# Performance work log

Hardware: AMD Instinct MI355X
Metric: run time of the kernel (lower is better)

The kernel has to match this reference:

```python
import jax, jax.numpy as jnp
import numpy as np

BS, H, NUM_JOB, NUM_OP, DK = 8, 16, 64, 64, 64
OPS_PER_JOB = 32
L = NUM_JOB * OPS_PER_JOB  # length_q = 2048; exactly L true slots per batch elem


def setup_inputs() -> dict:
    key = jax.random.key(0)
    k1, k2, k3 = jax.random.split(key, 3)
    q = jax.random.normal(k1, (BS, H, L, DK), dtype=jnp.float32)
    k = jax.random.normal(k2, (BS, H, L, DK), dtype=jnp.float32)
    v = jax.random.normal(k3, (BS, H, L, DK), dtype=jnp.float32)
    # ragged job->op mapping: first OPS_PER_JOB slots of each job are occupied
    op_mapping = jnp.tile((jnp.arange(NUM_OP) < OPS_PER_JOB)[None, None, :],
                          (BS, NUM_JOB, 1))  # (bs, num_job, num_op) bool
    # causal (lower-triangular) mask within each job
    tri = jnp.tril(jnp.ones((NUM_OP, NUM_OP), dtype=bool))
    triu_mask = jnp.tile(tri[None, None, :, :], (BS, NUM_JOB, 1, 1))
    return {"q": q, "k": k, "v": v, "op_mapping": op_mapping, "triu_mask": triu_mask}


def _rope_tables(num_op, dk):
    pos = jnp.arange(num_op, dtype=jnp.float32)
    i = jnp.arange(dk // 2, dtype=jnp.float32)
    theta = 1.0 / (10000.0 ** (2.0 * i / dk))
    ang = pos[:, None] * theta[None, :]                 # (num_op, dk/2)
    cos2 = jnp.repeat(jnp.cos(ang), 2, axis=-1)          # (num_op, dk) -> repeat_interleave(2)
    sin2 = jnp.repeat(jnp.sin(ang), 2, axis=-1)
    return cos2, sin2


def _rotate_half(x):
    xe = x[..., ::2]
    xo = x[..., 1::2]
    return jnp.stack([-xo, xe], axis=-1).reshape(x.shape)


def reference(q, k, v, op_mapping, triu_mask):
    bs, h, length_q, dk = q.shape
    _, num_job, num_op = op_mapping.shape
    flat_map = op_mapping.reshape(bs, num_job * num_op)  # (bs, J*O) bool
    # masked_scatter_ equivalent: true slot t (in flat row-major order) gets token cumsum-1
    pos = jnp.clip(jnp.cumsum(flat_map, axis=-1) - 1, 0, length_q - 1)  # (bs, J*O)
    idx = pos[:, None, :, None]  # broadcast over heads and dk

    def scatter_to_jobs(x):
        g = jnp.take_along_axis(x, idx, axis=2)                       # (bs,h,J*O,dk)
        g = jnp.where(flat_map[:, None, :, None], g, jnp.zeros((), x.dtype))
        return g.reshape(bs, h, num_job, num_op, dk)

    mq = scatter_to_jobs(q)
    mk = scatter_to_jobs(k)
    mv = scatter_to_jobs(v)

    # RoPE over the op axis
    cos2, sin2 = _rope_tables(num_op, dk)                             # (num_op, dk)
    mq = mq * cos2 + _rotate_half(mq) * sin2
    mk = mk * cos2 + _rotate_half(mk) * sin2

    score = jnp.einsum('bhjod,bhjpd->bhjop', mq, mk)                  # (bs,h,J,O,O)
    scale = 1.0 / jnp.sqrt(jnp.float32(dk))
    mask = triu_mask[:, None] & (score != 0)                          # compound mask
    s = jnp.where(mask, score * scale, -jnp.inf)
    invalid = jnp.sum(mask, axis=-1, keepdims=True) == 0              # empty rows
    s = jnp.where(invalid, jnp.float32(-1e9), s)
    w = jax.nn.softmax(s, axis=-1)
    out = jnp.einsum('bhjop,bhjpd->bhjod', w, mv)                     # (bs,h,J,O,dk)

    # gather back: out[matrix_mapping].reshape(bs,h,L,dk)
    out_flat = out.reshape(bs, h, num_job * num_op, dk)
    sel = jax.vmap(lambda m: jnp.nonzero(m, size=length_q)[0])(flat_map)  # (bs, L)
    tok = jnp.take_along_axis(out_flat, sel[:, None, :, None], axis=2)    # (bs,h,L,dk)
    # permute [0,2,1,3] then flatten heads: (bs, L, h*dk)
    return tok.transpose(0, 2, 1, 3).reshape(bs, length_q, h * dk)
```

## Files before the change

kernel.cpp:

```cpp
#include <hip/hip_runtime.h>
#include <hip/hip_bf16.h>


typedef _Float16 h8 __attribute__((ext_vector_type(8)));
typedef float f4 __attribute__((ext_vector_type(4)));
typedef unsigned short us8 __attribute__((ext_vector_type(8)));

__device__ __forceinline__ float bf2f(unsigned short u) {
    return __uint_as_float(((unsigned int)u) << 16);
}

__device__ __forceinline__ void load8f(const void* base, size_t idx, bool isbf, float o[8]) {
    if (isbf) {
        us8 v = *(const us8*)((const unsigned short*)base + idx);
#pragma unroll
        for (int t = 0; t < 8; ++t) o[t] = bf2f(v[t]);
    } else {
        const float* p = (const float*)base + idx;
        float4 a = *(const float4*)p;
        float4 b = *(const float4*)(p + 4);
        o[0] = a.x; o[1] = a.y; o[2] = a.z; o[3] = a.w;
        o[4] = b.x; o[5] = b.y; o[6] = b.z; o[7] = b.w;
    }
}

__device__ __forceinline__ float load1f(const void* base, size_t idx, bool isbf) {
    return isbf ? bf2f(((const unsigned short*)base)[idx])
                : ((const float*)base)[idx];
}

#define ROPE_LN_CONST 0.28782313662425575f

__global__ __launch_bounds__(256)
void attn_jobs(const void* __restrict__ qp, const void* __restrict__ kp,
               const void* __restrict__ vp, float* __restrict__ outp) {
    __shared__ float ps[4][32 * 33];

    const int tid  = threadIdx.x;
    const int wid  = tid >> 6;
    const int lane = tid & 63;
    const int lg   = lane >> 4;
    const int ln   = lane & 15;

    const int sub = blockIdx.x * 4 + wid;
    const int j = sub & 63;
    const int h = (sub >> 6) & 15;
    const int b = sub >> 10;

    unsigned int w0 = ((const unsigned int*)qp)[lane];
    unsigned int e8 = (w0 >> 7) & 0xFFu;
    bool hit = (e8 >= 96u) && (e8 <= 144u);
    const bool isbf = (__popcll(__ballot(hit)) >= 32);

    const size_t base = ((size_t)((b * 16 + h) * 2048 + j * 32)) * 64;

    h8 qf[2][2], kf[2][2];
#pragma unroll
    for (int ti = 0; ti < 2; ++ti) {
        const int r = ti * 16 + ln;
#pragma unroll
        for (int c = 0; c < 2; ++c) {
            const int dbase = c * 32 + lg * 8;
            float qa[8], ka[8];
            load8f(qp, base + (size_t)r * 64 + dbase, isbf, qa);
            load8f(kp, base + (size_t)r * 64 + dbase, isbf, ka);
#pragma unroll
            for (int t = 0; t < 4; ++t) {
                const int i = (dbase >> 1) + t;
                const float th = __expf(-(float)i * ROPE_LN_CONST);
                float sn, cs;
                __sincosf((float)r * th, &sn, &cs);
                const float qe = qa[2 * t], qo = qa[2 * t + 1];
                const float ke = ka[2 * t], ko = ka[2 * t + 1];
                qf[ti][c][2 * t]     = (_Float16)(qe * cs - qo * sn);
                qf[ti][c][2 * t + 1] = (_Float16)(qo * cs + qe * sn);
                kf[ti][c][2 * t]     = (_Float16)(ke * cs - ko * sn);
                kf[ti][c][2 * t + 1] = (_Float16)(ko * cs + ke * sn);
            }
        }
    }

    f4 sacc[2][2];
#pragma unroll
    for (int ti = 0; ti < 2; ++ti)
#pragma unroll
        for (int tj = 0; tj < 2; ++tj) {
            f4 acc = {0.f, 0.f, 0.f, 0.f};
            acc = __builtin_amdgcn_mfma_f32_16x16x32_f16(qf[ti][0], kf[tj][0], acc, 0, 0, 0);
            acc = __builtin_amdgcn_mfma_f32_16x16x32_f16(qf[ti][1], kf[tj][1], acc, 0, 0, 0);
            sacc[ti][tj] = acc;
        }

#pragma unroll
    for (int ti = 0; ti < 2; ++ti) {
#pragma unroll
        for (int reg = 0; reg < 4; ++reg) {
            const int row = ti * 16 + lg * 4 + reg;
            float s0 = sacc[ti][0][reg] * 0.125f;
            float s1 = sacc[ti][1][reg] * 0.125f;
            if (ln > row)      s0 = -INFINITY;
            if (16 + ln > row) s1 = -INFINITY;
            float m = fmaxf(s0, s1);
#pragma unroll
            for (int off = 8; off > 0; off >>= 1) m = fmaxf(m, __shfl_xor(m, off, 64));
            float p0 = __expf(s0 - m);
            float p1 = __expf(s1 - m);
            float l = p0 + p1;
#pragma unroll
            for (int off = 8; off > 0; off >>= 1) l += __shfl_xor(l, off, 64);
            const float linv = 1.0f / l;
            sacc[ti][0][reg] = p0 * linv;
            sacc[ti][1][reg] = p1 * linv;
        }
    }

    float* myps = ps[wid];
#pragma unroll
    for (int ti = 0; ti < 2; ++ti)
#pragma unroll
        for (int tj = 0; tj < 2; ++tj)
#pragma unroll
            for (int reg = 0; reg < 4; ++reg)
                myps[(ti * 16 + lg * 4 + reg) * 33 + tj * 16 + ln] = sacc[ti][tj][reg];
    __syncthreads();

    h8 paf[2];
#pragma unroll
    for (int ti = 0; ti < 2; ++ti)
#pragma unroll
        for (int t = 0; t < 8; ++t)
            paf[ti][t] = (_Float16)myps[(ti * 16 + ln) * 33 + lg * 8 + t];

    h8 vf[4];
#pragma unroll
    for (int tj = 0; tj < 4; ++tj)
#pragma unroll
        for (int t = 0; t < 8; ++t)
            vf[tj][t] = (_Float16)load1f(vp, base + (size_t)(lg * 8 + t) * 64 + tj * 16 + ln, isbf);

    f4 oacc[2][4];
#pragma unroll
    for (int ti = 0; ti < 2; ++ti)
#pragma unroll
        for (int tj = 0; tj < 4; ++tj) {
            f4 acc = {0.f, 0.f, 0.f, 0.f};
            oacc[ti][tj] = __builtin_amdgcn_mfma_f32_16x16x32_f16(paf[ti], vf[tj], acc, 0, 0, 0);
        }

#pragma unroll
    for (int ti = 0; ti < 2; ++ti)
#pragma unroll
        for (int reg = 0; reg < 4; ++reg) {
            const int row = ti * 16 + lg * 4 + reg;
            const size_t obase = ((size_t)b * 2048 + j * 32 + row) * 1024 + h * 64;
#pragma unroll
            for (int tj = 0; tj < 4; ++tj)
                outp[obase + tj * 16 + ln] = oacc[ti][tj][reg];
        }
}

extern "C" void kernel_launch(void* const* d_in, const int* in_sizes, int n_in,
                              void* d_out, int out_size, void* d_ws, size_t ws_size,
                              hipStream_t stream) {
    (void)in_sizes; (void)n_in; (void)d_ws; (void)ws_size; (void)out_size;
    const void* q = d_in[0];
    const void* k = d_in[1];
    const void* v = d_in[2];
    attn_jobs<<<2048, 256, 0, stream>>>(q, k, v, (float*)d_out);
}
```

Measured before the change: 225.6 us.

## Prefetch V before QK^T, store P as fp16 in LDS, drop block barrier

V is now loaded into raw registers before the QK^T MFMAs and softmax, so its global latency overlaps that compute instead of sitting after the softmax. The probability tile goes to LDS as fp16 with a padded stride, so each lane reads it back as a single vector of eight halves. The block-wide __syncthreads is replaced by a per-wave lgkmcnt wait, which relies on each wave using only its own LDS slice. Launch bounds request 4 blocks per CU and outputs are stored right after each MFMA, at the cost of 32 extra live registers for the prefetched V.

```diff
diff --git a/kernel.cpp b/kernel.cpp
--- a/kernel.cpp
+++ b/kernel.cpp
@@ -24,17 +24,12 @@
     }
 }
 
-__device__ __forceinline__ float load1f(const void* base, size_t idx, bool isbf) {
-    return isbf ? bf2f(((const unsigned short*)base)[idx])
-                : ((const float*)base)[idx];
-}
-
 #define ROPE_LN_CONST 0.28782313662425575f
 
-__global__ __launch_bounds__(256)
+__global__ __launch_bounds__(256, 4)
 void attn_jobs(const void* __restrict__ qp, const void* __restrict__ kp,
                const void* __restrict__ vp, float* __restrict__ outp) {
-    __shared__ float ps[4][32 * 33];
+    __shared__ alignas(16) _Float16 ps[4][32 * 40];
 
     const int tid  = threadIdx.x;
     const int wid  = tid >> 6;
@@ -49,8 +44,8 @@
 
     unsigned int w0 = ((const unsigned int*)qp)[lane];
     unsigned int e8 = (w0 >> 7) & 0xFFu;
-    bool hit = (e8 >= 96u) && (e8 <= 144u);
-    const bool isbf = (__popcll(__ballot(hit)) >= 32);
+    bool hitb = (e8 >= 96u) && (e8 <= 144u);
+    const bool isbf = (__popcll(__ballot(hitb)) >= 32);
 
     const size_t base = ((size_t)((b * 16 + h) * 2048 + j * 32)) * 64;
 
@@ -78,6 +73,23 @@
                 kf[ti][c][2 * t + 1] = (_Float16)(ko * cs + ke * sn);
             }
         }
+    }
+
+    unsigned int vr[32];
+    if (isbf) {
+#pragma unroll
+        for (int tj = 0; tj < 4; ++tj)
+#pragma unroll
+            for (int t = 0; t < 8; ++t)
+                vr[tj * 8 + t] = ((const unsigned short*)vp)
+                    [base + (size_t)(lg * 8 + t) * 64 + tj * 16 + ln];
+    } else {
+#pragma unroll
+        for (int tj = 0; tj < 4; ++tj)
+#pragma unroll
+            for (int t = 0; t < 8; ++t)
+                vr[tj * 8 + t] = ((const unsigned int*)vp)
+                    [base + (size_t)(lg * 8 + t) * 64 + tj * 16 + ln];
     }
 
     f4 sacc[2][2];
@@ -114,49 +126,52 @@
         }
     }
 
-    float* myps = ps[wid];
+    _Float16* myps = ps[wid];
 #pragma unroll
     for (int ti = 0; ti < 2; ++ti)
 #pragma unroll
         for (int tj = 0; tj < 2; ++tj)
 #pragma unroll
             for (int reg = 0; reg < 4; ++reg)
-                myps[(ti * 16 + lg * 4 + reg) * 33 + tj * 16 + ln] = sacc[ti][tj][reg];
-    __syncthreads();
+                myps[(ti * 16 + lg * 4 + reg) * 40 + tj * 16 + ln] =
+                    (_Float16)sacc[ti][tj][reg];
+
+    h8 vf[4];
+    if (isbf) {
+#pragma unroll
+        for (int tj = 0; tj < 4; ++tj)
+#pragma unroll
+            for (int t = 0; t < 8; ++t)
+                vf[tj][t] = (_Float16)bf2f((unsigned short)vr[tj * 8 + t]);
+    } else {
+#pragma unroll
+        for (int tj = 0; tj < 4; ++tj)
+#pragma unroll
+            for (int t = 0; t < 8; ++t)
+                vf[tj][t] = (_Float16)__uint_as_float(vr[tj * 8 + t]);
+    }
+
+    asm volatile("s_waitcnt lgkmcnt(0)" ::: "memory");
 
     h8 paf[2];
 #pragma unroll
     for (int ti = 0; ti < 2; ++ti)
+        paf[ti] = *(const h8*)&myps[(ti * 16 + ln) * 40 + lg * 8];
+
 #pragma unroll
-        for (int t = 0; t < 8; ++t)
-            paf[ti][t] = (_Float16)myps[(ti * 16 + ln) * 33 + lg * 8 + t];
-
-    h8 vf[4];
-#pragma unroll
-    for (int tj = 0; tj < 4; ++tj)
-#pragma unroll
-        for (int t = 0; t < 8; ++t)
-            vf[tj][t] = (_Float16)load1f(vp, base + (size_t)(lg * 8 + t) * 64 + tj * 16 + ln, isbf);
-
-    f4 oacc[2][4];
-#pragma unroll
-    for (int ti = 0; ti < 2; ++ti)
+    for (int ti = 0; ti < 2; ++ti) {
 #pragma unroll
         for (int tj = 0; tj < 4; ++tj) {
             f4 acc = {0.f, 0.f, 0.f, 0.f};
-            oacc[ti][tj] = __builtin_amdgcn_mfma_f32_16x16x32_f16(paf[ti], vf[tj], acc, 0, 0, 0);
+            acc = __builtin_amdgcn_mfma_f32_16x16x32_f16(paf[ti], vf[tj], acc, 0, 0, 0);
+#pragma unroll
+            for (int reg = 0; reg < 4; ++reg) {
+                const int row = ti * 16 + lg * 4 + reg;
+                outp[((size_t)b * 2048 + j * 32 + row) * 1024 + h * 64 + tj * 16 + ln] =
+                    acc[reg];
+            }
         }
-
-#pragma unroll
-    for (int ti = 0; ti < 2; ++ti)
-#pragma unroll
-        for (int reg = 0; reg < 4; ++reg) {
-            const int row = ti * 16 + lg * 4 + reg;
-            const size_t obase = ((size_t)b * 2048 + j * 32 + row) * 1024 + h * 64;
-#pragma unroll
-            for (int tj = 0; tj < 4; ++tj)
-                outp[obase + tj * 16 + ln] = oacc[ti][tj][reg];
-        }
+    }
 }
 
 extern "C" void kernel_launch(void* const* d_in, const int* in_sizes, int n_in,
```

Result: no change. 228.6 us (+1.3%).
